# Optimization experiments

Hardware: AMD Instinct MI355X
Metric: run time of the kernel (lower is better)

Reference implementation:

```python
import jax, jax.numpy as jnp
import numpy as np

DT = 0.01          # Euler step size
ALPHA = 1.0        # Grubb exponent (hardcoded in forward())
V0 = 0.02          # resting venous blood volume fraction
NOISE_AMP = 0.01   # amplitude of per-step noise injected into the neural drive
T = 1000           # integration length (hardcoded in forward())
B = 16384          # batch of independent simulations


def setup_inputs() -> dict:
    key = jax.random.key(0)
    noise = jax.random.normal(key, (T, B), dtype=jnp.float32)
    f32 = lambda v: jnp.asarray(v, dtype=jnp.float32)
    return {
        "noise": noise,
        "sigma": f32(0.9),
        "mu": f32(0.8),
        "lamb": f32(0.3),
        "beta": f32(0.9),
        "psi": f32(0.5),
        "phi": f32(2.0),
        "chi": f32(0.3),
    }


def reference(noise, sigma, mu, lamb, beta, psi, phi, chi):
    # Balloon-Windkessel BOLD model, explicit Euler, per-step noise.
    # States per simulation: s (vasodilatory signal), f (flow), v (volume), q (dHb).
    b = noise.shape[1]
    inv_alpha = 1.0 / ALPHA

    def step(carry, z):
        s, f, v, q = carry
        # oxygen extraction fraction E(f) = 1 - (1 - E0)^(1/f)
        E = 1.0 - (1.0 - beta) ** (1.0 / f)
        v_a = v ** inv_alpha  # outflow v^(1/alpha)
        s2 = s + DT * (NOISE_AMP * z - sigma * s - mu * (f - 1.0))
        f2 = f + DT * s
        v2 = v + DT * (f - v_a) / lamb
        q2 = q + DT * (f * E / beta - v_a * q / v) / lamb
        # BOLD readout at the new state
        y = V0 * (phi * (1.0 - q2) + psi * (1.0 - q2 / v2) + chi * (1.0 - v2))
        return (s2, f2, v2, q2), y

    init = (
        jnp.zeros((b,), noise.dtype),
        jnp.ones((b,), noise.dtype),
        jnp.ones((b,), noise.dtype),
        jnp.ones((b,), noise.dtype),
    )
    _, ys = jax.lax.scan(step, init, noise)  # ys: [T, B]
    return ys
```

## Files before the change

kernel.cpp:

```cpp
#include <hip/hip_runtime.h>


#define BATCH     16384
#define DT        0.01f
#define NOISE_AMP 0.01f
#define V0        0.02f
#define CHUNKS    20
#define CL        50
#define GSIMS     32
#define NTHREADS  (CHUNKS * GSIMS)

#if __has_builtin(__builtin_amdgcn_exp2f)
#define EXP2F(x) __builtin_amdgcn_exp2f(x)
#else
#define EXP2F(x) exp2f(x)
#endif

__device__ __forceinline__ float uf(float x) {
    return __uint_as_float(__builtin_amdgcn_readfirstlane(__float_as_uint(x)));
}

struct D22 { double a, b, c, d; };
__device__ __forceinline__ D22 dmul(D22 x, D22 y) {
    D22 r;
    r.a = x.a * y.a + x.b * y.c;  r.b = x.a * y.b + x.b * y.d;
    r.c = x.c * y.a + x.d * y.c;  r.d = x.c * y.b + x.d * y.d;
    return r;
}

__global__ __launch_bounds__(NTHREADS, 5) void balloon_scan(
    const float* __restrict__ noise,
    const float* __restrict__ p_sigma,
    const float* __restrict__ p_mu,
    const float* __restrict__ p_lamb,
    const float* __restrict__ p_beta,
    const float* __restrict__ p_psi,
    const float* __restrict__ p_phi,
    const float* __restrict__ p_chi,
    float* __restrict__ out)
{
    const int tid = threadIdx.x;
    const int g   = tid & (GSIMS - 1);
    const int cc  = tid >> 5;
    const int sim = blockIdx.x * GSIMS + g;

    const float sigma = uf(p_sigma[0]);
    const float mu    = uf(p_mu[0]);
    const float lamb  = uf(p_lamb[0]);
    const float beta  = uf(p_beta[0]);
    const float psi   = uf(p_psi[0]);
    const float phi   = uf(p_phi[0]);
    const float chi   = uf(p_chi[0]);

    const float as_   = 1.0f - DT * sigma;
    const float dtn   = DT * NOISE_AMP;
    const float dtm   = DT * mu;
    const float dt_il = uf((float)(0.01 / (double)lamb));
    const float av    = 1.0f - dt_il;
    const float kq    = uf(dt_il / beta);
    const float lc    = uf(log2f(1.0f - beta));
    const float c0 = V0 * (phi + psi + chi), c1 = V0 * phi, c2 = V0 * psi, c3 = V0 * chi;

    D22 A; A.a = 1.0 - 0.01 * (double)sigma; A.b = -0.01 * (double)mu;
           A.c = 0.01;                       A.d = 1.0;
    D22 A2 = dmul(A, A), A4 = dmul(A2, A2), A8 = dmul(A4, A4);
    D22 A16 = dmul(A8, A8), A32 = dmul(A16, A16);
    D22 P = dmul(dmul(A32, A16), A2);
    double avd = 1.0 - 0.01 / (double)lamb;
    double av2 = avd * avd, av4 = av2 * av2, av8 = av4 * av4;
    double av16 = av8 * av8, av32 = av16 * av16;
    double ap = av32 * av16 * av2;

    float M11[5], M12[5], M21[5], M22[5], AVP[5];
#pragma unroll
    for (int j = 0; j < 5; ++j) {
        M11[j] = uf((float)P.a); M12[j] = uf((float)P.b);
        M21[j] = uf((float)P.c); M22[j] = uf((float)P.d);
        AVP[j] = uf((float)ap);
        P = dmul(P, P); ap = ap * ap;
    }

    float ws = 0.0f, wf = 1.0f, avc = 1.0f;
#pragma unroll
    for (int j = 0; j < 5; ++j) {
        if ((cc >> j) & 1) {
            float t = __builtin_fmaf(M11[j], ws, M12[j] * wf);
            wf = __builtin_fmaf(M21[j], ws, M22[j] * wf);
            ws = t;
            avc *= AVP[j];
        }
    }

    __shared__ float sA[NTHREADS];
    __shared__ float sB[NTHREADS];

    const float* zp = noise + cc * (CL * BATCH) + sim;

    float rs = 0.0f, rf = 0.0f;
#pragma unroll 10
    for (int j = 0; j < CL; ++j) {
        const float z = zp[j * BATCH];
        const float u = __builtin_fmaf(dtn, z, dtm);
        const float t = __builtin_fmaf(as_, rs, __builtin_fmaf(-dtm, rf, u));
        rf = __builtin_fmaf(DT, rs, rf);
        rs = t;
    }

    sA[tid] = rs; sB[tid] = rf;
    __syncthreads();
#pragma unroll
    for (int j = 0; j < 5; ++j) {
        const int off = 1 << j;
        float ns = 0.0f, nf = 0.0f;
        const bool has = (cc >= off);
        if (has) { ns = sA[tid - off * GSIMS]; nf = sB[tid - off * GSIMS]; }
        __syncthreads();
        if (has) {
            rs = __builtin_fmaf(M11[j], ns, __builtin_fmaf(M12[j], nf, rs));
            rf = __builtin_fmaf(M21[j], ns, __builtin_fmaf(M22[j], nf, rf));
            sA[tid] = rs; sB[tid] = rf;
        }
        __syncthreads();
    }
    float s0 = ws, f0 = wf;
    if (cc > 0) { s0 += sA[tid - GSIMS]; f0 += sB[tid - GSIMS]; }
    __syncthreads();

    float s = s0, f = f0, Rv = 0.0f, Rq = 0.0f;
#pragma unroll 10
    for (int j = 0; j < CL; ++j) {
        const float z    = zp[j * BATCH];
        const float invf = __builtin_amdgcn_rcpf(f);
        const float e2   = EXP2F(lc * invf);
        const float t1   = __builtin_fmaf(-f, e2, f);
        Rv = __builtin_fmaf(av, Rv, dt_il * f);
        Rq = __builtin_fmaf(av, Rq, kq * t1);
        const float s2 = __builtin_fmaf(as_, s,
                         __builtin_fmaf(dtn, z,
                         __builtin_fmaf(-dtm, f, dtm)));
        f = __builtin_fmaf(DT, s, f);
        s = s2;
    }

    sA[tid] = Rv; sB[tid] = Rq;
    __syncthreads();
#pragma unroll
    for (int j = 0; j < 5; ++j) {
        const int off = 1 << j;
        float nv = 0.0f, nq = 0.0f;
        const bool has = (cc >= off);
        if (has) { nv = sA[tid - off * GSIMS]; nq = sB[tid - off * GSIMS]; }
        __syncthreads();
        if (has) {
            Rv = __builtin_fmaf(AVP[j], nv, Rv);
            Rq = __builtin_fmaf(AVP[j], nq, Rq);
            sA[tid] = Rv; sB[tid] = Rq;
        }
        __syncthreads();
    }
    float v = avc, q = avc;
    if (cc > 0) { v += sA[tid - GSIMS]; q += sB[tid - GSIMS]; }

    s = s0; f = f0;
    float* op = out + cc * (CL * BATCH) + sim;
#pragma unroll 10
    for (int j = 0; j < CL; ++j) {
        const float z    = zp[j * BATCH];
        const float invf = __builtin_amdgcn_rcpf(f);
        const float e2   = EXP2F(lc * invf);
        const float t1   = __builtin_fmaf(-f, e2, f);
        const float vn   = __builtin_fmaf(av, v, dt_il * f);
        const float qn   = __builtin_fmaf(av, q, kq * t1);
        const float s2 = __builtin_fmaf(as_, s,
                         __builtin_fmaf(dtn, z,
                         __builtin_fmaf(-dtm, f, dtm)));
        f = __builtin_fmaf(DT, s, f);
        s = s2;

        const float invv = __builtin_amdgcn_rcpf(vn);
        const float y = __builtin_fmaf(-c2, qn * invv,
                        __builtin_fmaf(-c3, vn,
                        __builtin_fmaf(-c1, qn, c0)));
        op[j * BATCH] = y;
        v = vn; q = qn;
    }
}

extern "C" void kernel_launch(void* const* d_in, const int* in_sizes, int n_in,
                              void* d_out, int out_size, void* d_ws, size_t ws_size,
                              hipStream_t stream) {
    const float* noise   = (const float*)d_in[0];
    const float* p_sigma = (const float*)d_in[1];
    const float* p_mu    = (const float*)d_in[2];
    const float* p_lamb  = (const float*)d_in[3];
    const float* p_beta  = (const float*)d_in[4];
    const float* p_psi   = (const float*)d_in[5];
    const float* p_phi   = (const float*)d_in[6];
    const float* p_chi   = (const float*)d_in[7];

    balloon_scan<<<BATCH / GSIMS, NTHREADS, 0, stream>>>(
        noise, p_sigma, p_mu, p_lamb, p_beta, p_psi, p_phi, p_chi,
        (float*)d_out);
}
```

Before: 142.1 us.

## Cache noise and flow in registers, double chunk count with narrower groups

```diff
diff --git a/kernel.cpp b/kernel.cpp
--- a/kernel.cpp
+++ b/kernel.cpp
@@ -5,10 +5,11 @@
 #define DT        0.01f
 #define NOISE_AMP 0.01f
 #define V0        0.02f
-#define CHUNKS    20
-#define CL        50
-#define GSIMS     32
+#define CHUNKS    40
+#define CL        25
+#define GSIMS     16
 #define NTHREADS  (CHUNKS * GSIMS)
+#define LEVELS    6
 
 #if __has_builtin(__builtin_amdgcn_exp2f)
 #define EXP2F(x) __builtin_amdgcn_exp2f(x)
@@ -28,7 +29,7 @@
     return r;
 }
 
-__global__ __launch_bounds__(NTHREADS, 5) void balloon_scan(
+__global__ __launch_bounds__(NTHREADS, 6) void balloon_scan(
     const float* __restrict__ noise,
     const float* __restrict__ p_sigma,
     const float* __restrict__ p_mu,
@@ -41,7 +42,7 @@
 {
     const int tid = threadIdx.x;
     const int g   = tid & (GSIMS - 1);
-    const int cc  = tid >> 5;
+    const int cc  = tid >> 4;
     const int sim = blockIdx.x * GSIMS + g;
 
     const float sigma = uf(p_sigma[0]);
@@ -64,16 +65,16 @@
     D22 A; A.a = 1.0 - 0.01 * (double)sigma; A.b = -0.01 * (double)mu;
            A.c = 0.01;                       A.d = 1.0;
     D22 A2 = dmul(A, A), A4 = dmul(A2, A2), A8 = dmul(A4, A4);
-    D22 A16 = dmul(A8, A8), A32 = dmul(A16, A16);
-    D22 P = dmul(dmul(A32, A16), A2);
+    D22 A16 = dmul(A8, A8);
+    D22 P = dmul(dmul(A16, A8), A);
     double avd = 1.0 - 0.01 / (double)lamb;
     double av2 = avd * avd, av4 = av2 * av2, av8 = av4 * av4;
-    double av16 = av8 * av8, av32 = av16 * av16;
-    double ap = av32 * av16 * av2;
-
-    float M11[5], M12[5], M21[5], M22[5], AVP[5];
-#pragma unroll
-    for (int j = 0; j < 5; ++j) {
+    double av16 = av8 * av8;
+    double ap = av16 * av8 * avd;
+
+    float M11[LEVELS], M12[LEVELS], M21[LEVELS], M22[LEVELS], AVP[LEVELS];
+#pragma unroll
+    for (int j = 0; j < LEVELS; ++j) {
         M11[j] = uf((float)P.a); M12[j] = uf((float)P.b);
         M21[j] = uf((float)P.c); M22[j] = uf((float)P.d);
         AVP[j] = uf((float)ap);
@@ -82,7 +83,7 @@
 
     float ws = 0.0f, wf = 1.0f, avc = 1.0f;
 #pragma unroll
-    for (int j = 0; j < 5; ++j) {
+    for (int j = 0; j < LEVELS; ++j) {
         if ((cc >> j) & 1) {
             float t = __builtin_fmaf(M11[j], ws, M12[j] * wf);
             wf = __builtin_fmaf(M21[j], ws, M22[j] * wf);
@@ -96,11 +97,15 @@
 
     const float* zp = noise + cc * (CL * BATCH) + sim;
 
+    float zr[CL];
+#pragma unroll
+    for (int j = 0; j < CL; ++j)
+        zr[j] = __builtin_nontemporal_load(&zp[j * BATCH]);
+
     float rs = 0.0f, rf = 0.0f;
-#pragma unroll 10
+#pragma unroll
     for (int j = 0; j < CL; ++j) {
-        const float z = zp[j * BATCH];
-        const float u = __builtin_fmaf(dtn, z, dtm);
+        const float u = __builtin_fmaf(dtn, zr[j], dtm);
         const float t = __builtin_fmaf(as_, rs, __builtin_fmaf(-dtm, rf, u));
         rf = __builtin_fmaf(DT, rs, rf);
         rs = t;
@@ -109,7 +114,7 @@
     sA[tid] = rs; sB[tid] = rf;
     __syncthreads();
 #pragma unroll
-    for (int j = 0; j < 5; ++j) {
+    for (int j = 0; j < LEVELS; ++j) {
         const int off = 1 << j;
         float ns = 0.0f, nf = 0.0f;
         const bool has = (cc >= off);
@@ -127,16 +132,17 @@
     __syncthreads();
 
     float s = s0, f = f0, Rv = 0.0f, Rq = 0.0f;
-#pragma unroll 10
+#pragma unroll
     for (int j = 0; j < CL; ++j) {
-        const float z    = zp[j * BATCH];
+        const float zf   = zr[j];
         const float invf = __builtin_amdgcn_rcpf(f);
         const float e2   = EXP2F(lc * invf);
         const float t1   = __builtin_fmaf(-f, e2, f);
         Rv = __builtin_fmaf(av, Rv, dt_il * f);
         Rq = __builtin_fmaf(av, Rq, kq * t1);
+        zr[j] = f;
         const float s2 = __builtin_fmaf(as_, s,
-                         __builtin_fmaf(dtn, z,
+                         __builtin_fmaf(dtn, zf,
                          __builtin_fmaf(-dtm, f, dtm)));
         f = __builtin_fmaf(DT, s, f);
         s = s2;
@@ -145,7 +151,7 @@
     sA[tid] = Rv; sB[tid] = Rq;
     __syncthreads();
 #pragma unroll
-    for (int j = 0; j < 5; ++j) {
+    for (int j = 0; j < LEVELS; ++j) {
         const int off = 1 << j;
         float nv = 0.0f, nq = 0.0f;
         const bool has = (cc >= off);
@@ -161,27 +167,20 @@
     float v = avc, q = avc;
     if (cc > 0) { v += sA[tid - GSIMS]; q += sB[tid - GSIMS]; }
 
-    s = s0; f = f0;
     float* op = out + cc * (CL * BATCH) + sim;
-#pragma unroll 10
+#pragma unroll
     for (int j = 0; j < CL; ++j) {
-        const float z    = zp[j * BATCH];
-        const float invf = __builtin_amdgcn_rcpf(f);
+        const float fj   = zr[j];
+        const float invf = __builtin_amdgcn_rcpf(fj);
         const float e2   = EXP2F(lc * invf);
-        const float t1   = __builtin_fmaf(-f, e2, f);
-        const float vn   = __builtin_fmaf(av, v, dt_il * f);
+        const float t1   = __builtin_fmaf(-fj, e2, fj);
+        const float vn   = __builtin_fmaf(av, v, dt_il * fj);
         const float qn   = __builtin_fmaf(av, q, kq * t1);
-        const float s2 = __builtin_fmaf(as_, s,
-                         __builtin_fmaf(dtn, z,
-                         __builtin_fmaf(-dtm, f, dtm)));
-        f = __builtin_fmaf(DT, s, f);
-        s = s2;
-
         const float invv = __builtin_amdgcn_rcpf(vn);
         const float y = __builtin_fmaf(-c2, qn * invv,
                         __builtin_fmaf(-c3, vn,
                         __builtin_fmaf(-c1, qn, c0)));
-        op[j * BATCH] = y;
+        __builtin_nontemporal_store(y, &op[j * BATCH]);
         v = vn; q = qn;
     }
 }
```

Result: slower. 163.9 us (+15.3%).
